# Optimization experiments

Measured on AMD Instinct MI355X. Metric: run time of the kernel, lower is better.

Reference implementation:

```python
import jax, jax.numpy as jnp
from jax import lax
import numpy as np

PARAM_NAMES = ['S1_max','S2_max','f_tens','f_rchr','f_base','r1','ku','c','alpha','psi','kappa','ki','ks','n','v','v_A','v_B','Ac_max','b','lambda','chi','mu_t','T_rain','T_melt','melt_rate','lapse_rate','opg','MFMAX','MFMIN']
PARAM_BOUNDS = {'S1_max':(50.,5000.),'S2_max':(100.,10000.),'f_tens':(.05,.95),'f_rchr':(.05,.95),'f_base':(.05,.95),'r1':(.05,.95),'ku':(.01,1000.),'c':(1.,20.),'alpha':(1.,250.),'psi':(1.,5.),'kappa':(.05,.95),'ki':(.01,1000.),'ks':(.001,10000.),'n':(1.,10.),'v':(.001,.25),'v_A':(.001,.25),'v_B':(.001,.25),'Ac_max':(.05,.95),'b':(.001,3.),'lambda':(5.,10.),'chi':(2.,5.),'mu_t':(.01,5.),'T_rain':(-2.,4.),'T_melt':(-2.,4.),'melt_rate':(1.,10.),'lapse_rate':(-9.8,0.),'opg':(0.,1.),'MFMAX':(1.,10.),'MFMIN':(0.,10.)}
_LOW = jnp.asarray(np.array([PARAM_BOUNDS[n][0] for n in PARAM_NAMES], np.float32))
_HIGH = jnp.asarray(np.array([PARAM_BOUNDS[n][1] for n in PARAM_NAMES], np.float32))
_IDX = {n: i for i, n in enumerate(PARAM_NAMES)}
REF_ELEV = 1500.0      # reference gauge elevation [m]
ROUTE_SHAPE = 2.5      # gamma unit-hydrograph shape
UH_LEN = 30            # routing kernel length [days]


def setup_inputs() -> dict:
    key = jax.random.key(0)
    k1, k2, k3 = jax.random.split(key, 3)
    E, T, NB = 64, 8192, 16
    raw_params = 0.5 * jax.random.normal(k1, (E, 29), jnp.float32)
    u = jax.random.uniform(k2, (T, 3), jnp.float32)
    precip = jnp.where(u[:, 0] > 0.6, (u[:, 0] - 0.6) * 50.0, 0.0)  # mm/day
    pet = u[:, 1] * 5.0                                             # mm/day
    temp = (u[:, 2] - 0.4) * 25.0                                   # deg C
    forcing = jnp.stack([precip, pet, temp], axis=1)
    state_init = jnp.array([50.0, 250.0], jnp.float32)
    af = jax.random.uniform(k3, (NB,), jnp.float32) + 0.1
    area_frac = af / af.sum()
    mean_elev = 800.0 + 150.0 * jnp.arange(NB, dtype=jnp.float32)
    return dict(raw_params=raw_params, forcing=forcing, state_init=state_init,
                area_frac=area_frac, mean_elev=mean_elev)


def _simulate(raw_params, forcing, state_init, area_frac, mean_elev):
    phys = _LOW + (_HIGH - _LOW) * jax.nn.sigmoid(raw_params)  # [E,29] sigmoid-bounded params
    g = lambda n: phys[:, _IDX[n]][:, None]                    # [E,1]
    s1max, s2max = g('S1_max'), g('S2_max')
    ku, c_exp, ki = g('ku'), g('c'), g('ki')
    ks, n_exp = g('ks')[:, 0], g('n')[:, 0]
    ac_max, b_exp = g('Ac_max'), g('b')
    t_rain, t_melt, melt_rate = g('T_rain'), g('T_melt'), g('melt_rate')
    delev = (mean_elev - REF_ELEV) / 1000.0                    # [nb] km
    tshift = g('lapse_rate') * delev                           # [E,nb]
    pmult = jnp.maximum(1.0 + g('opg') * delev, 0.0)           # [E,nb]
    s2max1 = g('S2_max')[:, 0]
    E, NB = raw_params.shape[0], mean_elev.shape[0]

    swe0 = jnp.zeros((E, NB), phys.dtype)
    s1_0 = jnp.broadcast_to(state_init[0], (E, NB))
    s2_0 = jnp.broadcast_to(state_init[1], (E,))

    def step(carry, x):
        swe, s1, s2 = carry
        p, pet, tair = x[0], x[1], x[2]
        tb = tair + tshift                                     # band temperature [E,nb]
        pb = p * pmult                                         # band precip
        rain = jnp.where(tb > t_rain, pb, 0.0)
        snow = pb - rain
        melt = jnp.minimum(melt_rate * jnp.maximum(tb - t_melt, 0.0), swe + snow)
        swe = swe + snow - melt
        infl = rain + melt
        w1 = jnp.clip(s1 / s1max, 0.0, 1.0)
        evap = pet * w1
        qsx = ac_max * w1 ** b_exp * infl                      # saturated-area runoff
        perc = ku * w1 ** c_exp                                # percolation to lower zone
        qif = ki * w1                                          # interflow
        s1n = s1 + infl - qsx - evap - perc - qif
        over1 = jnp.maximum(s1n - s1max, 0.0)
        s1 = jnp.clip(s1n, 0.0, s1max)
        qsurf = qsx + over1
        rech = jnp.sum(area_frac * perc, axis=-1)              # [E]
        w2 = jnp.clip(s2 / s2max1, 0.0, 1.0)
        qb = ks * w2 ** n_exp                                  # baseflow
        s2n = s2 + rech - qb
        over2 = jnp.maximum(s2n - s2max1, 0.0)
        s2 = jnp.clip(s2n, 0.0, s2max1)
        q = jnp.sum(area_frac * (qsurf + qif), axis=-1) + qb + over2
        return (swe, s1, s2), q

    _, runoff = lax.scan(step, (swe0, s1_0, s2_0), forcing)   # [T,E]
    runoff = runoff.T                                          # [E,T]

    # gamma unit-hydrograph routing: shape=ROUTE_SHAPE, scale=mu_t
    delay = phys[:, _IDX['mu_t']]                              # [E]
    tmid = jnp.arange(UH_LEN, dtype=runoff.dtype) + 0.5        # bin midpoints [days]
    k = jnp.asarray(ROUTE_SHAPE, runoff.dtype)
    logpdf = ((k - 1.0) * jnp.log(tmid)[None, :]
              - tmid[None, :] / delay[:, None]
              - lax.lgamma(k) - k * jnp.log(delay)[:, None])
    w = jnp.exp(logpdf)
    w = w / w.sum(axis=1, keepdims=True)                       # [E,UH_LEN]
    T = runoff.shape[1]
    padded = jnp.pad(runoff, ((0, 0), (UH_LEN - 1, 0)))
    routed = jnp.zeros_like(runoff)
    for l in range(UH_LEN):  # small fixed kernel loop (not a data-dim loop)
        routed = routed + w[:, l:l + 1] * lax.dynamic_slice_in_dim(padded, UH_LEN - 1 - l, T, axis=1)
    return routed


def reference(raw_params, forcing, state_init, area_frac, mean_elev):
    return _simulate(raw_params, forcing, state_init, area_frac, mean_elev)
```

## Files before the change

### kernel.cpp

```cpp
#include <hip/hip_runtime.h>
#include <math.h>

#define T_STEPS 8192
#define GROUP   64
#define NQ      (GROUP / 4)
#define NG      (T_STEPS / GROUP)
#define UH      30

__device__ __forceinline__ float hw_exp2(float x) { return __builtin_amdgcn_exp2f(x); }
__device__ __forceinline__ float hw_log2(float x) { return __builtin_amdgcn_logf(x); }

#if __has_builtin(__builtin_amdgcn_fmed3f)
__device__ __forceinline__ float clamp01(float x) { return __builtin_amdgcn_fmed3f(x, 0.0f, 1.0f); }
#else
__device__ __forceinline__ float clamp01(float x) { return fminf(fmaxf(x, 0.0f), 1.0f); }
#endif

__global__ __launch_bounds__(320, 1) void fuse_pipe_kernel(
    const float* __restrict__ raw,
    const float* __restrict__ forcing,
    const float* __restrict__ state_init,
    const float* __restrict__ area_frac,
    const float* __restrict__ mean_elev,
    float* __restrict__ routed)
{
    const int tid  = threadIdx.x;
    const int wid  = tid >> 6;
    const int lane = tid & 63;
    const int grp  = lane >> 4;
    const int nb   = lane & 15;
    const int e    = blockIdx.x * 4 + grp;

    __shared__ float4 bufI4[2][NQ][64];
    __shared__ float4 bufC4[2][NQ][64];
    __shared__ float4 bufP4[2][NQ][67];
    __shared__ float4 bufQ4[2][NQ][67];
    __shared__ float4 bufR4[2][4][NQ + 1];
    __shared__ float4 bufS4[2][4][NQ + 1];
    __shared__ float qring[4][257];

    for (int k = tid; k < 4 * 257; k += 320)
        ((float*)qring)[k] = 0.0f;

    const float* rp = raw + e * 29;
    auto phys = [&](int idx, float lo, float hi) {
        float x = rp[idx];
        float s = 1.0f / (1.0f + expf(-x));
        return lo + (hi - lo) * s;
    };
    const float s1max = phys(0,  50.0f,  5000.0f);
    const float s2max = phys(1,  100.0f, 10000.0f);
    const float ku    = phys(6,  0.01f,  1000.0f);
    const float c_exp = phys(7,  1.0f,   20.0f);
    const float ki    = phys(11, 0.01f,  1000.0f);
    const float ks    = phys(12, 0.001f, 10000.0f);
    const float n_exp = phys(13, 1.0f,   10.0f);
    const float acmax = phys(17, 0.05f,  0.95f);
    const float b_exp = phys(18, 0.001f, 3.0f);
    const float train = phys(22, -2.0f,  4.0f);
    const float tmelt = phys(23, -2.0f,  4.0f);
    const float mrate = phys(24, 1.0f,   10.0f);
    const float lapse = phys(25, -9.8f,  0.0f);
    const float opg   = phys(26, 0.0f,   1.0f);

    const float delev  = (mean_elev[nb] - 1500.0f) / 1000.0f;
    const float tshift = lapse * delev;
    const float pmult  = fmaxf(1.0f + opg * delev, 0.0f);
    const float af     = area_frac[nb];
    const float inv_s1max = 1.0f / s1max;
    const float inv_s2max = 1.0f / s2max;
    const float kup    = ku * inv_s1max;
    const float ksn    = ks * inv_s2max;
    const float afku   = af * ku;
    const float afki   = af * ki;
    const float afs1   = af * s1max;

    float swe = 0.0f;
    float w1  = state_init[0] * inv_s1max;
    float v2  = state_init[1] * inv_s2max;

    float wloc[UH];
    if (wid == 4) {
        const float x     = raw[e * 29 + 21];
        const float sig   = 1.0f / (1.0f + expf(-x));
        const float delay = 0.01f + (5.0f - 0.01f) * sig;
        const float lgd   = logf(delay);
        const float invd  = 1.0f / delay;
        float s = 0.0f;
        #pragma unroll
        for (int l = 0; l < UH; ++l) {
            const float tm = (float)l + 0.5f;
            const float lp = 1.5f * logf(tm) - tm * invd
                           - 0.28468287047291918f - 2.5f * lgd;
            wloc[l] = expf(lp);
            s += wloc[l];
        }
        const float inv = 1.0f / s;
        #pragma unroll
        for (int l = 0; l < UH; ++l) wloc[l] *= inv;
    }

    float* __restrict__ out = routed + (size_t)e * T_STEPS;
    const float4* __restrict__ fvec = (const float4*)forcing;

    for (int i = 0; i < NG + 5; ++i) {
        if (wid == 0) {
            if (i < NG) {
                const int pb_ = i & 1;
                const int base = i * 48;
                #pragma unroll
                for (int h = 0; h < 4; ++h) {
                    float f[48];
                    #pragma unroll
                    for (int j = 0; j < 12; ++j) {
                        const float4 L = fvec[base + h * 12 + j];
                        f[4*j+0] = L.x; f[4*j+1] = L.y; f[4*j+2] = L.z; f[4*j+3] = L.w;
                    }
                    float4 vi, vc;
                    #pragma unroll
                    for (int s = 0; s < 16; ++s) {
                        const int tt = h * 16 + s;
                        const float p    = f[3*s + 0];
                        const float pet  = f[3*s + 1];
                        const float tair = f[3*s + 2];
                        const float tb   = tair + tshift;
                        const float pcp  = p * pmult;
                        const float snow = (tb > train) ? 0.0f : pcp;
                        const float ssn  = swe + snow;
                        const float mcap = mrate * fmaxf(tb - tmelt, 0.0f);
                        const float swen = fmaxf(ssn - mcap, 0.0f);
                        const float infl = pcp + swe - swen;
                        swe = swen;
                        const int c3 = tt & 3;
                        (&vi.x)[c3] = infl * inv_s1max;
                        (&vc.x)[c3] = fmaf(-(pet + ki), inv_s1max, 1.0f);
                        if (c3 == 3) {
                            bufI4[pb_][tt >> 2][lane] = vi;
                            bufC4[pb_][tt >> 2][lane] = vc;
                        }
                    }
                }
            }
        } else if (wid == 1) {
            const int g = i - 1;
            if (g >= 0 && g < NG) {
                const int pb_ = g & 1;
                float4 fi4[NQ], fc4[NQ];
                #pragma unroll
                for (int k = 0; k < NQ; ++k) {
                    fi4[k] = bufI4[pb_][k][lane];
                    fc4[k] = bufC4[pb_][k][lane];
                }
                #pragma unroll
                for (int k = 0; k < NQ; ++k) {
                    float4 oP, oQ;
                    #pragma unroll
                    for (int c3 = 0; c3 < 4; ++c3) {
                        const float fi  = (&fi4[k].x)[c3];
                        const float fcv = (&fc4[k].x)[c3];
                        const float fap = acmax * fi;
                        const float lg  = hw_log2(w1);
                        const float pwc = hw_exp2(c_exp * lg);
                        const float pwb = hw_exp2(b_exp * lg);
                        const float u   = fmaf(fcv, w1, fi);
                        const float u1  = fmaf(-kup, pwc, u);
                        const float u2  = fmaf(-fap, pwb, u1);
                        const float over1 = fmaxf(u2 - 1.0f, 0.0f);
                        const float qift  = afki * w1;
                        w1 = clamp01(u2);
                        const float qsxn = fap * pwb;
                        (&oP.x)[c3] = afku * pwc;
                        (&oQ.x)[c3] = fmaf(afs1, qsxn + over1, qift);
                    }
                    bufP4[pb_][k][lane] = oP;
                    bufQ4[pb_][k][lane] = oQ;
                }
            }
        } else if (wid == 2) {
            const int g = i - 2;
            if (g >= 0 && g < NG) {
                const int pb_ = g & 1;
                const int arr = lane >> 5;
                const int se  = (lane >> 3) & 3;
                const int tq  = lane & 7;
                #pragma unroll
                for (int j = 0; j < 2; ++j) {
                    const int q_ = tq + 8 * j;
                    const float4* src = arr ? &bufQ4[pb_][q_][se * 16]
                                            : &bufP4[pb_][q_][se * 16];
                    float4 s = src[0];
                    #pragma unroll
                    for (int n = 1; n < 16; ++n) {
                        const float4 v = src[n];
                        s.x += v.x; s.y += v.y; s.z += v.z; s.w += v.w;
                    }
                    if (arr) bufS4[pb_][se][q_] = s;
                    else     bufR4[pb_][se][q_] = s;
                }
            }
        } else if (wid == 3) {
            const int g = i - 3;
            if (g >= 0 && g < NG) {
                const int pb_ = g & 1;
                const int slot = (g & 3) * 64;
                float qk0 = 0.0f, qk1 = 0.0f, qk2 = 0.0f, qk3 = 0.0f;
                auto c2body = [&](bool clampPw) {
                    #pragma unroll
                    for (int k = 0; k < NQ; ++k) {
                        const float4 r4 = bufR4[pb_][grp][k];
                        const float4 s4 = bufS4[pb_][grp][k];
                        #pragma unroll
                        for (int c3 = 0; c3 < 4; ++c3) {
                            const int tt = 4 * k + c3;
                            const float rech = (&r4.x)[c3];
                            const float qsum = (&s4.x)[c3];
                            const float lg2 = hw_log2(v2);
                            float m = n_exp * lg2;
                            if (clampPw) m = fminf(m, 0.0f);
                            const float pwm = hw_exp2(m);
                            const float u   = fmaf(rech, inv_s2max, v2);
                            const float u2  = fmaf(-ksn, pwm, u);
                            const float over2 = fmaxf(u2 - 1.0f, 0.0f);
                            v2 = clamp01(u2);
                            const float q = fmaf(s2max, over2, fmaf(ks, pwm, qsum));
                            const bool sel = (tt & 15) == nb;
                            if      (tt < 16) qk0 = sel ? q : qk0;
                            else if (tt < 32) qk1 = sel ? q : qk1;
                            else if (tt < 48) qk2 = sel ? q : qk2;
                            else              qk3 = sel ? q : qk3;
                        }
                    }
                };
                if (g == 0) c2body(true); else c2body(false);

                qring[grp][slot + nb]      = qk0;
                qring[grp][slot + nb + 16] = qk1;
                qring[grp][slot + nb + 32] = qk2;
                qring[grp][slot + nb + 48] = qk3;
            }
        } else {
            const int g = i - 5;
            if (g >= 0 && g < NG) {
                const int base = (g & 3) * 64;
                #pragma unroll
                for (int j = 0; j < 4; ++j) {
                    const int pl = nb + 16 * j;
                    float acc = 0.0f;
                    #pragma unroll
                    for (int l = 0; l < UH; ++l) {
                        const int idx = (base + pl - l) & 255;
                        acc = fmaf(wloc[l], qring[grp][idx], acc);
                    }
                    out[g * GROUP + pl] = acc;
                }
            }
        }
        __syncthreads();
    }
}

extern "C" void kernel_launch(void* const* d_in, const int* in_sizes, int n_in,
                              void* d_out, int out_size, void* d_ws, size_t ws_size,
                              hipStream_t stream) {
    const float* raw        = (const float*)d_in[0];
    const float* forcing    = (const float*)d_in[1];
    const float* state_init = (const float*)d_in[2];
    const float* area_frac  = (const float*)d_in[3];
    const float* mean_elev  = (const float*)d_in[4];

    float* out = (float*)d_out;

    fuse_pipe_kernel<<<16, 320, 0, stream>>>(raw, forcing, state_init,
                                             area_frac, mean_elev, out);
}
```

Baseline: 339.9 us.

## Merge snow and soil-1 pipeline stages into one wave with register prefetch

The separate snow/forcing stage and upper-soil stage are fused into a single wavefront, so the intermediate LDS buffers for infiltration and coefficients are no longer needed. The pipeline drops from five waves to four and from 133 to 132 barrier-separated iterations. Forcing loads are double-buffered in registers, prefetching the next chunk while the current one is computed, to hide global load latency. In exchange, wave 0 now runs both serial recurrences back to back, which lengthens the critical per-iteration stage and may slow every barrier step.

```diff
diff --git a/kernel.cpp b/kernel.cpp
--- a/kernel.cpp
+++ b/kernel.cpp
@@ -16,7 +16,7 @@
 __device__ __forceinline__ float clamp01(float x) { return fminf(fmaxf(x, 0.0f), 1.0f); }
 #endif
 
-__global__ __launch_bounds__(320, 1) void fuse_pipe_kernel(
+__global__ __launch_bounds__(256, 1) void fuse_pipe_kernel(
     const float* __restrict__ raw,
     const float* __restrict__ forcing,
     const float* __restrict__ state_init,
@@ -31,15 +31,13 @@
     const int nb   = lane & 15;
     const int e    = blockIdx.x * 4 + grp;
 
-    __shared__ float4 bufI4[2][NQ][64];
-    __shared__ float4 bufC4[2][NQ][64];
     __shared__ float4 bufP4[2][NQ][67];
     __shared__ float4 bufQ4[2][NQ][67];
     __shared__ float4 bufR4[2][4][NQ + 1];
     __shared__ float4 bufS4[2][4][NQ + 1];
     __shared__ float qring[4][257];
 
-    for (int k = tid; k < 4 * 257; k += 320)
+    for (int k = tid; k < 4 * 257; k += 256)
         ((float*)qring)[k] = 0.0f;
 
     const float* rp = raw + e * 29;
@@ -80,7 +78,7 @@
     float v2  = state_init[1] * inv_s2max;
 
     float wloc[UH];
-    if (wid == 4) {
+    if (wid == 3) {
         const float x     = raw[e * 29 + 21];
         const float sig   = 1.0f / (1.0f + expf(-x));
         const float delay = 0.01f + (5.0f - 0.01f) * sig;
@@ -103,26 +101,32 @@
     float* __restrict__ out = routed + (size_t)e * T_STEPS;
     const float4* __restrict__ fvec = (const float4*)forcing;
 
-    for (int i = 0; i < NG + 5; ++i) {
+    float4 fb[2][12];
+    if (wid == 0) {
+        #pragma unroll
+        for (int j = 0; j < 12; ++j) fb[0][j] = fvec[j];
+    }
+
+    for (int i = 0; i < NG + 4; ++i) {
         if (wid == 0) {
             if (i < NG) {
                 const int pb_ = i & 1;
-                const int base = i * 48;
                 #pragma unroll
                 for (int h = 0; h < 4; ++h) {
-                    float f[48];
-                    #pragma unroll
-                    for (int j = 0; j < 12; ++j) {
-                        const float4 L = fvec[base + h * 12 + j];
-                        f[4*j+0] = L.x; f[4*j+1] = L.y; f[4*j+2] = L.z; f[4*j+3] = L.w;
-                    }
-                    float4 vi, vc;
+                    const int cur = h & 1, nxt = cur ^ 1;
+                    {
+                        int nh = h + 1, ng = i;
+                        if (nh == 4) { nh = 0; ng = (i + 1 < NG) ? i + 1 : NG - 1; }
+                        const float4* s4 = fvec + (ng * 48 + nh * 12);
+                        #pragma unroll
+                        for (int j = 0; j < 12; ++j) fb[nxt][j] = s4[j];
+                    }
+                    float4 oP, oQ;
                     #pragma unroll
                     for (int s = 0; s < 16; ++s) {
-                        const int tt = h * 16 + s;
-                        const float p    = f[3*s + 0];
-                        const float pet  = f[3*s + 1];
-                        const float tair = f[3*s + 2];
+                        const float p    = (&fb[cur][(3*s    ) >> 2].x)[(3*s    ) & 3];
+                        const float pet  = (&fb[cur][(3*s + 1) >> 2].x)[(3*s + 1) & 3];
+                        const float tair = (&fb[cur][(3*s + 2) >> 2].x)[(3*s + 2) & 3];
                         const float tb   = tair + tshift;
                         const float pcp  = p * pmult;
                         const float snow = (tb > train) ? 0.0f : pcp;
@@ -131,33 +135,8 @@
                         const float swen = fmaxf(ssn - mcap, 0.0f);
                         const float infl = pcp + swe - swen;
                         swe = swen;
-                        const int c3 = tt & 3;
-                        (&vi.x)[c3] = infl * inv_s1max;
-                        (&vc.x)[c3] = fmaf(-(pet + ki), inv_s1max, 1.0f);
-                        if (c3 == 3) {
-                            bufI4[pb_][tt >> 2][lane] = vi;
-                            bufC4[pb_][tt >> 2][lane] = vc;
-                        }
-                    }
-                }
-            }
-        } else if (wid == 1) {
-            const int g = i - 1;
-            if (g >= 0 && g < NG) {
-                const int pb_ = g & 1;
-                float4 fi4[NQ], fc4[NQ];
-                #pragma unroll
-                for (int k = 0; k < NQ; ++k) {
-                    fi4[k] = bufI4[pb_][k][lane];
-                    fc4[k] = bufC4[pb_][k][lane];
-                }
-                #pragma unroll
-                for (int k = 0; k < NQ; ++k) {
-                    float4 oP, oQ;
-                    #pragma unroll
-                    for (int c3 = 0; c3 < 4; ++c3) {
-                        const float fi  = (&fi4[k].x)[c3];
-                        const float fcv = (&fc4[k].x)[c3];
+                        const float fi  = infl * inv_s1max;
+                        const float fcv = fmaf(-(pet + ki), inv_s1max, 1.0f);
                         const float fap = acmax * fi;
                         const float lg  = hw_log2(w1);
                         const float pwc = hw_exp2(c_exp * lg);
@@ -169,15 +148,22 @@
                         const float qift  = afki * w1;
                         w1 = clamp01(u2);
                         const float qsxn = fap * pwb;
+                        const int tt = h * 16 + s, c3 = tt & 3;
                         (&oP.x)[c3] = afku * pwc;
                         (&oQ.x)[c3] = fmaf(afs1, qsxn + over1, qift);
-                    }
-                    bufP4[pb_][k][lane] = oP;
-                    bufQ4[pb_][k][lane] = oQ;
+                        if (c3 == 3) {
+                            bufP4[pb_][tt >> 2][lane] = oP;
+                            bufQ4[pb_][tt >> 2][lane] = oQ;
+                        }
+                    }
+                    #pragma unroll
+                    for (int j = 0; j < 12; ++j)
+                        asm volatile("" : "+v"(fb[nxt][j].x), "+v"(fb[nxt][j].y),
+                                          "+v"(fb[nxt][j].z), "+v"(fb[nxt][j].w));
                 }
             }
-        } else if (wid == 2) {
-            const int g = i - 2;
+        } else if (wid == 1) {
+            const int g = i - 1;
             if (g >= 0 && g < NG) {
                 const int pb_ = g & 1;
                 const int arr = lane >> 5;
@@ -198,8 +184,8 @@
                     else     bufR4[pb_][se][q_] = s;
                 }
             }
-        } else if (wid == 3) {
-            const int g = i - 3;
+        } else if (wid == 2) {
+            const int g = i - 2;
             if (g >= 0 && g < NG) {
                 const int pb_ = g & 1;
                 const int slot = (g & 3) * 64;
@@ -239,7 +225,7 @@
                 qring[grp][slot + nb + 48] = qk3;
             }
         } else {
-            const int g = i - 5;
+            const int g = i - 4;
             if (g >= 0 && g < NG) {
                 const int base = (g & 3) * 64;
                 #pragma unroll
@@ -270,6 +256,6 @@
 
     float* out = (float*)d_out;
 
-    fuse_pipe_kernel<<<16, 320, 0, stream>>>(raw, forcing, state_init,
+    fuse_pipe_kernel<<<16, 256, 0, stream>>>(raw, forcing, state_init,
                                              area_frac, mean_elev, out);
 }
```

New measurement: 547.9 us. 1.61x slower.
